# Optimization experiments

Measured on AMD Instinct MI355X. Metric: run time of the kernel, lower is better.

## Reference

```python
import jax, jax.numpy as jnp
import numpy as np

NUM_USERS = 120000
NUM_ITEMS = 30000
NUM_NODES = NUM_USERS + NUM_ITEMS
EMBED_DIM = 64
N_LAYERS = 3
N_EDGES = 4000000


def setup_inputs() -> dict:
    key = jax.random.key(0)
    k_emb, k_row, k_col = jax.random.split(key, 3)
    row = jax.random.randint(k_row, (N_EDGES,), 0, NUM_NODES, dtype=jnp.int32)
    col = jax.random.randint(k_col, (N_EDGES,), 0, NUM_NODES, dtype=jnp.int32)
    # symmetric normalization weights: D^{-1/2}[row] * D^{-1/2}[col]
    deg = jnp.bincount(row, length=NUM_NODES).astype(jnp.float32)
    deg_inv_sqrt = jnp.where(deg > 0, deg ** -0.5, 0.0)
    edge_weight = deg_inv_sqrt[row] * deg_inv_sqrt[col]
    emb = 0.1 * jax.random.normal(k_emb, (NUM_NODES, EMBED_DIM), dtype=jnp.float32)
    return {"emb": emb, "edge_weight": edge_weight, "row": row, "col": col}


def reference(emb, edge_weight, row, col):
    # one LightGCN propagation: out[row] += edge_weight * x[col]  (SpMM)
    def propagate(x):
        msg = x[col] * edge_weight[:, None]            # [E, D] gather + scale
        return jax.ops.segment_sum(msg, row, num_segments=NUM_NODES)  # scatter-add

    out = emb
    xk = emb
    for _ in range(N_LAYERS):
        xk = propagate(xk)
        out = out + xk
    out = out / (N_LAYERS + 1)
    user_emb = out[:NUM_USERS]
    item_emb = out[NUM_USERS:]
    return (user_emb, item_emb)
```

## Files before the change

### kernel.cpp

```cpp
#include <hip/hip_runtime.h>

#define NUM_USERS 120000
#define NUM_ITEMS 30000
#define NUM_NODES 150000
#define EMBED_DIM 64
#define N_LAYERS 3
#define N_EDGES 4000000

#define BW_SHIFT 9
#define BW_ROWS (1 << BW_SHIFT)
#define BW_MASK (BW_ROWS - 1)
#define NBUCK ((NUM_NODES + BW_MASK) >> BW_SHIFT)
#define BUCK_CAP 16000
#define SUB_E 8192

typedef unsigned short us8v __attribute__((ext_vector_type(8)));


__device__ __forceinline__ float bf2f(unsigned short u) {
    union { unsigned int i; float f; } v;
    v.i = ((unsigned int)u) << 16;
    return v.f;
}
__device__ __forceinline__ unsigned short f2bf(float f) {
    union { float f; unsigned int i; } v;
    v.f = f;
    unsigned int u = v.i;
    u += 0x7FFFu + ((u >> 16) & 1u);
    return (unsigned short)(u >> 16);
}


__global__ void zero_ints(int* __restrict__ p, int n) {
    int i = blockIdx.x * blockDim.x + threadIdx.x;
    int stride = gridDim.x * blockDim.x;
    for (; i < n; i += stride) p[i] = 0;
}

__global__ void conv_u0(const float4* __restrict__ emb,
                        const int* __restrict__ rs,
                        ushort4* __restrict__ u0, int n4) {
    int i = blockIdx.x * blockDim.x + threadIdx.x;
    int stride = gridDim.x * blockDim.x;
    for (; i < n4; i += stride) {
        int node = i >> 4;
        int deg = rs[node + 1] - rs[node];
        float dinv = (deg > 0) ? rsqrtf((float)deg) : 0.f;
        float4 v = emb[i];
        ushort4 q;
        q.x = f2bf(v.x * dinv); q.y = f2bf(v.y * dinv);
        q.z = f2bf(v.z * dinv); q.w = f2bf(v.w * dinv);
        u0[i] = q;
    }
}


__global__ void __launch_bounds__(256)
bucket_bin2(const int* __restrict__ row, const int* __restrict__ col,
            int* __restrict__ gcnt, int* __restrict__ stage, int nEdges) {
    __shared__ int lbuf[SUB_E];
    __shared__ int ldst[SUB_E];
    __shared__ int hist[NBUCK];
    __shared__ int cur[NBUCK];
    __shared__ int dlt[NBUCK];
    __shared__ int s0[512], s1[512];

    int nSub = (nEdges + SUB_E - 1) / SUB_E;
    for (int s = blockIdx.x; s < nSub; s += gridDim.x) {
        int e0 = s * SUB_E;
        int n = nEdges - e0; if (n > SUB_E) n = SUB_E;

        for (int j = threadIdx.x; j < NBUCK; j += 256) hist[j] = 0;
        __syncthreads();
        for (int i = threadIdx.x; i < n; i += 256)
            atomicAdd(&hist[row[e0 + i] >> BW_SHIFT], 1);
        __syncthreads();

        for (int j = threadIdx.x; j < 512; j += 256)
            s0[j] = (j < NBUCK) ? hist[j] : 0;
        __syncthreads();
        int *a = s0, *bb = s1;
        for (int off = 1; off < 512; off <<= 1) {
            for (int j = threadIdx.x; j < 512; j += 256) {
                int x = a[j];
                if (j >= off) x += a[j - off];
                bb[j] = x;
            }
            __syncthreads();
            int* t = a; a = bb; bb = t;
        }
        for (int j = threadIdx.x; j < NBUCK; j += 256) {
            int c = hist[j];
            int ls = j ? a[j - 1] : 0;
            cur[j] = ls;
            int g = c ? atomicAdd(&gcnt[j], c) : 0;
            dlt[j] = j * BUCK_CAP + g - ls;
        }
        __syncthreads();
        for (int i = threadIdx.x; i < n; i += 256) {
            int r = row[e0 + i];
            int b = r >> BW_SHIFT;
            int lpos = atomicAdd(&cur[b], 1);
            lbuf[lpos] = ((r & BW_MASK) << 18) | col[e0 + i];
            int d = dlt[b] + lpos;
            ldst[lpos] = (d - b * BUCK_CAP < BUCK_CAP) ? d : -1;
        }
        __syncthreads();
        for (int j = threadIdx.x; j < n; j += 256) {
            int d = ldst[j];
            if (d >= 0) stage[d] = lbuf[j];
        }
        __syncthreads();
    }
}

__global__ void bucket_scan(const int* __restrict__ gcnt, int* __restrict__ bstart,
                            int* __restrict__ rs) {
    __shared__ int s0[512], s1[512];
    int tid = threadIdx.x;
    int v = 0;
    if (tid < NBUCK) { v = gcnt[tid]; if (v > BUCK_CAP) v = BUCK_CAP; }
    s0[tid] = v;
    __syncthreads();
    int* a = s0; int* bb = s1;
    for (int off = 1; off < 512; off <<= 1) {
        int x = a[tid];
        if (tid >= off) x += a[tid - off];
        bb[tid] = x;
        __syncthreads();
        int* t = a; a = bb; bb = t;
    }
    if (tid == 0) bstart[0] = 0;
    if (tid < NBUCK) bstart[tid + 1] = a[tid];
    if (tid == 0) rs[NUM_NODES] = a[NBUCK - 1];
}

__global__ void __launch_bounds__(256)
bucket_scatter(const int* __restrict__ stage, const int* __restrict__ gcnt,
               const int* __restrict__ bstart, int* __restrict__ rs,
               int* __restrict__ csr) {
    __shared__ int s0[BW_ROWS], s1[BW_ROWS];
    int b = blockIdx.x;
    int tid = threadIdx.x;
    int nrec = gcnt[b]; if (nrec > BUCK_CAP) nrec = BUCK_CAP;
    int base = bstart[b];
    const int* st = stage + (size_t)b * BUCK_CAP;
    int baseRow = b << BW_SHIFT;
    int rows = NUM_NODES - baseRow; if (rows > BW_ROWS) rows = BW_ROWS;

    for (int j = tid; j < BW_ROWS; j += 256) s0[j] = 0;
    __syncthreads();
    for (int i = tid; i < nrec; i += 256) atomicAdd(&s0[st[i] >> 18], 1);
    __syncthreads();

    int* a = s0; int* bb = s1;
    for (int off = 1; off < BW_ROWS; off <<= 1) {
        for (int j = tid; j < BW_ROWS; j += 256) {
            int x = a[j];
            if (j >= off) x += a[j - off];
            bb[j] = x;
        }
        __syncthreads();
        int* t = a; a = bb; bb = t;
    }

    for (int r = tid; r < rows; r += 256)
        rs[baseRow + r] = base + (r ? a[r - 1] : 0);

    for (int j = tid; j < BW_ROWS; j += 256) bb[j] = 0;
    __syncthreads();
    for (int i = tid; i < nrec; i += 256) {
        int rec = st[i];
        int r = rec >> 18;
        int rank = atomicAdd(&bb[r], 1);
        csr[base + (r ? a[r - 1] : 0) + rank] = rec & 0x3FFFF;
    }
}

__global__ void __launch_bounds__(256)
lgcn_prop_u(const us8v* __restrict__ xb,
            const int* __restrict__ rs,
            const int* __restrict__ csr,
            us8v* __restrict__ yb, int nNodes) {
    int gtid = blockIdx.x * blockDim.x + threadIdx.x;
    int node = gtid >> 3;
    int sub  = threadIdx.x & 7;
    if (node >= nNodes) return;
    int s = rs[node], e = rs[node + 1];
    float acc[8] = {0.f, 0.f, 0.f, 0.f, 0.f, 0.f, 0.f, 0.f};

    int base = s;
    for (; base + 8 <= e; base += 8) {
        int c8 = csr[base + sub];
        us8v v[8];
#pragma unroll
        for (int j = 0; j < 8; ++j) {
            int bc = __shfl(c8, j, 8);
            v[j] = xb[(size_t)bc * 8 + sub];
        }
#pragma unroll
        for (int j = 0; j < 8; ++j)
#pragma unroll
            for (int k = 0; k < 8; ++k)
                acc[k] += bf2f(v[j][k]);
    }
    if (base < e) {
        int nn = e - base;
        int idx = base + sub;
        int c8 = (idx < e) ? csr[idx] : 0;
        us8v v[7];
#pragma unroll
        for (int j = 0; j < 7; ++j) {
            int bc = __shfl(c8, j, 8);
            v[j] = xb[(size_t)bc * 8 + sub];
        }
#pragma unroll
        for (int j = 0; j < 7; ++j) {
            float m = (j < nn) ? 1.f : 0.f;
#pragma unroll
            for (int k = 0; k < 8; ++k)
                acc[k] = fmaf(bf2f(v[j][k]), m, acc[k]);
        }
    }

    int deg = e - s;
    float dinv = (deg > 0) ? rsqrtf((float)deg) : 0.f;
    float d2 = dinv * dinv;
    us8v q;
#pragma unroll
    for (int k = 0; k < 8; ++k) q[k] = f2bf(acc[k] * d2);
    yb[(size_t)node * 8 + sub] = q;
}

__global__ void lgcn_fuse(const float4* __restrict__ emb,
                          const ushort4* __restrict__ u1,
                          const ushort4* __restrict__ u2,
                          const ushort4* __restrict__ u3,
                          const int* __restrict__ rs,
                          float4* __restrict__ out, int n4) {
    int i = blockIdx.x * blockDim.x + threadIdx.x;
    int stride = gridDim.x * blockDim.x;
    const float quart = 1.0f / (N_LAYERS + 1);
    for (; i < n4; i += stride) {
        int node = i >> 4;
        int deg = rs[node + 1] - rs[node];
        float sd = (deg > 0) ? sqrtf((float)deg) : 0.f;
        ushort4 a = u1[i], b = u2[i], c = u3[i];
        float4 ev = emb[i];
        float4 o;
        o.x = (ev.x + (bf2f(a.x) + bf2f(b.x) + bf2f(c.x)) * sd) * quart;
        o.y = (ev.y + (bf2f(a.y) + bf2f(b.y) + bf2f(c.y)) * sd) * quart;
        o.z = (ev.z + (bf2f(a.z) + bf2f(b.z) + bf2f(c.z)) * sd) * quart;
        o.w = (ev.w + (bf2f(a.w) + bf2f(b.w) + bf2f(c.w)) * sd) * quart;
        out[i] = o;
    }
}


__global__ void lgcn_init(const float4* __restrict__ emb,
                          float4* __restrict__ x,
                          float4* __restrict__ out, int n4) {
    int i = blockIdx.x * blockDim.x + threadIdx.x;
    int stride = gridDim.x * blockDim.x;
    for (; i < n4; i += stride) {
        float4 v = emb[i];
        x[i] = v;
        out[i] = v;
    }
}

__global__ void lgcn_zero(float4* __restrict__ y, int n4) {
    int i = blockIdx.x * blockDim.x + threadIdx.x;
    int stride = gridDim.x * blockDim.x;
    float4 z = make_float4(0.f, 0.f, 0.f, 0.f);
    for (; i < n4; i += stride) y[i] = z;
}

__global__ void lgcn_edge(const float* __restrict__ x,
                          const float* __restrict__ w,
                          const int* __restrict__ row,
                          const int* __restrict__ col,
                          float* __restrict__ y, int nEdges) {
    int tid = blockIdx.x * blockDim.x + threadIdx.x;
    int wave = tid >> 6;
    int lane = threadIdx.x & 63;
    int nWaves = (gridDim.x * blockDim.x) >> 6;
    for (int e = wave; e < nEdges; e += nWaves) {
        int r = row[e];
        int c = col[e];
        float wt = w[e];
        float v = x[(size_t)c * EMBED_DIM + lane] * wt;
        atomicAdd(&y[(size_t)r * EMBED_DIM + lane], v);
    }
}

__global__ void lgcn_accum(const float4* __restrict__ y,
                           float4* __restrict__ out, float scale, int n4) {
    int i = blockIdx.x * blockDim.x + threadIdx.x;
    int stride = gridDim.x * blockDim.x;
    for (; i < n4; i += stride) {
        float4 o = out[i];
        float4 v = y[i];
        o.x = (o.x + v.x) * scale;
        o.y = (o.y + v.y) * scale;
        o.z = (o.z + v.z) * scale;
        o.w = (o.w + v.w) * scale;
        out[i] = o;
    }
}


extern "C" void kernel_launch(void* const* d_in, const int* in_sizes, int n_in,
                              void* d_out, int out_size, void* d_ws, size_t ws_size,
                              hipStream_t stream) {
    const float* emb = (const float*)d_in[0];
    const float* ew  = (const float*)d_in[1];
    const int*   row = (const int*)d_in[2];
    const int*   col = (const int*)d_in[3];
    float* out = (float*)d_out;

    const size_t tableElems = (size_t)NUM_NODES * EMBED_DIM;
    const int n4 = (int)(tableElems / 4);

    char* ws = (char*)d_ws;
    size_t off = 0;
    auto alloc = [&](size_t bytes) {
        char* p = ws + off;
        off += (bytes + 255) & ~(size_t)255;
        return p;
    };
    ushort4* u1b   = (ushort4*)alloc(tableElems * 2);
    ushort4* u2b   = (ushort4*)alloc(tableElems * 2);
    ushort4* u3b   = (ushort4*)alloc(tableElems * 2);
    int*     csr   = (int*)    alloc((size_t)N_EDGES * 4);
    char*    stg0  = alloc(tableElems * 2 > (size_t)NBUCK * BUCK_CAP * 4
                               ? tableElems * 2
                               : (size_t)NBUCK * BUCK_CAP * 4);
    int*     rs    = (int*)    alloc((size_t)(NUM_NODES + 32) * 4);
    int*     bstart= (int*)    alloc((size_t)(NBUCK + 8) * 4);
    int*     gcnt  = (int*)    alloc((size_t)(NBUCK + 8) * 4);
    size_t need = off;
    int*     stage = (int*)stg0;
    ushort4* u0b   = (ushort4*)stg0;

    if (ws_size >= need) {
        zero_ints<<<2, 256, 0, stream>>>(gcnt, NBUCK);
        bucket_bin2<<<512, 256, 0, stream>>>(row, col, gcnt, stage, N_EDGES);
        bucket_scan<<<1, 512, 0, stream>>>(gcnt, bstart, rs);
        bucket_scatter<<<NBUCK, 256, 0, stream>>>(stage, gcnt, bstart, rs, csr);

        conv_u0<<<2048, 256, 0, stream>>>((const float4*)emb, rs,
                                          (ushort4*)u0b, n4);

        const int propBlocks = (NUM_NODES * 8 + 255) / 256;
        lgcn_prop_u<<<propBlocks, 256, 0, stream>>>((const us8v*)u0b, rs, csr,
                                                    (us8v*)u1b, NUM_NODES);
        lgcn_prop_u<<<propBlocks, 256, 0, stream>>>((const us8v*)u1b, rs, csr,
                                                    (us8v*)u2b, NUM_NODES);
        lgcn_prop_u<<<propBlocks, 256, 0, stream>>>((const us8v*)u2b, rs, csr,
                                                    (us8v*)u3b, NUM_NODES);

        lgcn_fuse<<<2048, 256, 0, stream>>>((const float4*)emb,
                                            u1b, u2b, u3b, rs,
                                            (float4*)out, n4);
    } else {
        float* x = (float*)d_ws;
        float* y = x + tableElems;
        lgcn_init<<<2048, 256, 0, stream>>>((const float4*)emb, (float4*)x,
                                            (float4*)out, n4);
        for (int l = 0; l < N_LAYERS; ++l) {
            lgcn_zero<<<2048, 256, 0, stream>>>((float4*)y, n4);
            lgcn_edge<<<4096, 256, 0, stream>>>(x, ew, row, col, y, N_EDGES);
            float scale = (l == N_LAYERS - 1) ? 1.0f / (N_LAYERS + 1) : 1.0f;
            lgcn_accum<<<2048, 256, 0, stream>>>((const float4*)y, (float4*)out,
                                                 scale, n4);
            float* t = x; x = y; y = t;
        }
    }
}
```

Baseline: 336.9 us.

## Fuse bf16 conversion into CSR scatter and final combine into last propagation

Folds the emb-to-bf16 pre-scaling into the bucket_scatter kernel, reusing the per-row degrees already held in shared memory, which removes the separate conv_u0 launch and its extra read of rs. The last propagation layer now computes the final weighted sum of emb, u1, u2 and the fresh layer output directly, which drops the lgcn_fuse kernel and the write and re-read of the u3 table. It also adds a launch_bounds occupancy hint and replaces rsqrt squared with a reciprocal. In exchange, staging no longer aliases u0, so the workspace grows.

Result: no change. 334.1 us (-0.8%).

```diff
diff --git a/kernel.cpp b/kernel.cpp
--- a/kernel.cpp
+++ b/kernel.cpp
@@ -35,23 +35,6 @@
     int i = blockIdx.x * blockDim.x + threadIdx.x;
     int stride = gridDim.x * blockDim.x;
     for (; i < n; i += stride) p[i] = 0;
-}
-
-__global__ void conv_u0(const float4* __restrict__ emb,
-                        const int* __restrict__ rs,
-                        ushort4* __restrict__ u0, int n4) {
-    int i = blockIdx.x * blockDim.x + threadIdx.x;
-    int stride = gridDim.x * blockDim.x;
-    for (; i < n4; i += stride) {
-        int node = i >> 4;
-        int deg = rs[node + 1] - rs[node];
-        float dinv = (deg > 0) ? rsqrtf((float)deg) : 0.f;
-        float4 v = emb[i];
-        ushort4 q;
-        q.x = f2bf(v.x * dinv); q.y = f2bf(v.y * dinv);
-        q.z = f2bf(v.z * dinv); q.w = f2bf(v.w * dinv);
-        u0[i] = q;
-    }
 }
 
 
@@ -138,7 +121,8 @@
 __global__ void __launch_bounds__(256)
 bucket_scatter(const int* __restrict__ stage, const int* __restrict__ gcnt,
                const int* __restrict__ bstart, int* __restrict__ rs,
-               int* __restrict__ csr) {
+               int* __restrict__ csr,
+               const float4* __restrict__ emb4, ushort4* __restrict__ u0) {
     __shared__ int s0[BW_ROWS], s1[BW_ROWS];
     int b = blockIdx.x;
     int tid = threadIdx.x;
@@ -175,13 +159,29 @@
         int rank = atomicAdd(&bb[r], 1);
         csr[base + (r ? a[r - 1] : 0) + rank] = rec & 0x3FFFF;
     }
-}
-
-__global__ void __launch_bounds__(256)
+
+    for (int i = tid; i < rows * 16; i += 256) {
+        int rl = i >> 4;
+        int deg = a[rl] - (rl ? a[rl - 1] : 0);
+        float dinv = (deg > 0) ? rsqrtf((float)deg) : 0.f;
+        int g = baseRow * 16 + i;
+        float4 v = emb4[g];
+        ushort4 q;
+        q.x = f2bf(v.x * dinv); q.y = f2bf(v.y * dinv);
+        q.z = f2bf(v.z * dinv); q.w = f2bf(v.w * dinv);
+        u0[g] = q;
+    }
+}
+
+template <int FINAL>
+__global__ void __launch_bounds__(256, 3)
 lgcn_prop_u(const us8v* __restrict__ xb,
             const int* __restrict__ rs,
             const int* __restrict__ csr,
-            us8v* __restrict__ yb, int nNodes) {
+            us8v* __restrict__ yb,
+            const us8v* __restrict__ u1,
+            const float4* __restrict__ emb,
+            float4* __restrict__ out, int nNodes) {
     int gtid = blockIdx.x * blockDim.x + threadIdx.x;
     int node = gtid >> 3;
     int sub  = threadIdx.x & 7;
@@ -224,35 +224,36 @@
     }
 
     int deg = e - s;
-    float dinv = (deg > 0) ? rsqrtf((float)deg) : 0.f;
-    float d2 = dinv * dinv;
-    us8v q;
-#pragma unroll
-    for (int k = 0; k < 8; ++k) q[k] = f2bf(acc[k] * d2);
-    yb[(size_t)node * 8 + sub] = q;
-}
-
-__global__ void lgcn_fuse(const float4* __restrict__ emb,
-                          const ushort4* __restrict__ u1,
-                          const ushort4* __restrict__ u2,
-                          const ushort4* __restrict__ u3,
-                          const int* __restrict__ rs,
-                          float4* __restrict__ out, int n4) {
-    int i = blockIdx.x * blockDim.x + threadIdx.x;
-    int stride = gridDim.x * blockDim.x;
-    const float quart = 1.0f / (N_LAYERS + 1);
-    for (; i < n4; i += stride) {
-        int node = i >> 4;
-        int deg = rs[node + 1] - rs[node];
+    float d2 = (deg > 0) ? 1.0f / (float)deg : 0.f;
+    size_t o8 = (size_t)node * 8 + sub;
+
+    if (FINAL == 0) {
+        us8v q;
+#pragma unroll
+        for (int k = 0; k < 8; ++k) q[k] = f2bf(acc[k] * d2);
+        yb[o8] = q;
+    } else {
         float sd = (deg > 0) ? sqrtf((float)deg) : 0.f;
-        ushort4 a = u1[i], b = u2[i], c = u3[i];
-        float4 ev = emb[i];
-        float4 o;
-        o.x = (ev.x + (bf2f(a.x) + bf2f(b.x) + bf2f(c.x)) * sd) * quart;
-        o.y = (ev.y + (bf2f(a.y) + bf2f(b.y) + bf2f(c.y)) * sd) * quart;
-        o.z = (ev.z + (bf2f(a.z) + bf2f(b.z) + bf2f(c.z)) * sd) * quart;
-        o.w = (ev.w + (bf2f(a.w) + bf2f(b.w) + bf2f(c.w)) * sd) * quart;
-        out[i] = o;
+        const float quart = 1.0f / (N_LAYERS + 1);
+        us8v a1 = u1[o8];
+        us8v a2 = xb[o8];
+        float sum[8];
+#pragma unroll
+        for (int k = 0; k < 8; ++k)
+            sum[k] = bf2f(a1[k]) + bf2f(a2[k]) + acc[k] * d2;
+        size_t o4 = o8 * 2;
+        float4 e0 = emb[o4], e1 = emb[o4 + 1];
+        float4 r0, r1;
+        r0.x = (e0.x + sum[0] * sd) * quart;
+        r0.y = (e0.y + sum[1] * sd) * quart;
+        r0.z = (e0.z + sum[2] * sd) * quart;
+        r0.w = (e0.w + sum[3] * sd) * quart;
+        r1.x = (e1.x + sum[4] * sd) * quart;
+        r1.y = (e1.y + sum[5] * sd) * quart;
+        r1.z = (e1.z + sum[6] * sd) * quart;
+        r1.w = (e1.w + sum[7] * sd) * quart;
+        out[o4] = r0;
+        out[o4 + 1] = r1;
     }
 }
 
@@ -329,40 +330,33 @@
         off += (bytes + 255) & ~(size_t)255;
         return p;
     };
+    ushort4* u0b   = (ushort4*)alloc(tableElems * 2);
     ushort4* u1b   = (ushort4*)alloc(tableElems * 2);
     ushort4* u2b   = (ushort4*)alloc(tableElems * 2);
-    ushort4* u3b   = (ushort4*)alloc(tableElems * 2);
     int*     csr   = (int*)    alloc((size_t)N_EDGES * 4);
-    char*    stg0  = alloc(tableElems * 2 > (size_t)NBUCK * BUCK_CAP * 4
-                               ? tableElems * 2
-                               : (size_t)NBUCK * BUCK_CAP * 4);
+    int*     stage = (int*)    alloc((size_t)NBUCK * BUCK_CAP * 4);
     int*     rs    = (int*)    alloc((size_t)(NUM_NODES + 32) * 4);
     int*     bstart= (int*)    alloc((size_t)(NBUCK + 8) * 4);
     int*     gcnt  = (int*)    alloc((size_t)(NBUCK + 8) * 4);
     size_t need = off;
-    int*     stage = (int*)stg0;
-    ushort4* u0b   = (ushort4*)stg0;
 
     if (ws_size >= need) {
         zero_ints<<<2, 256, 0, stream>>>(gcnt, NBUCK);
         bucket_bin2<<<512, 256, 0, stream>>>(row, col, gcnt, stage, N_EDGES);
         bucket_scan<<<1, 512, 0, stream>>>(gcnt, bstart, rs);
-        bucket_scatter<<<NBUCK, 256, 0, stream>>>(stage, gcnt, bstart, rs, csr);
-
-        conv_u0<<<2048, 256, 0, stream>>>((const float4*)emb, rs,
-                                          (ushort4*)u0b, n4);
+        bucket_scatter<<<NBUCK, 256, 0, stream>>>(stage, gcnt, bstart, rs, csr,
+                                                  (const float4*)emb, u0b);
 
         const int propBlocks = (NUM_NODES * 8 + 255) / 256;
-        lgcn_prop_u<<<propBlocks, 256, 0, stream>>>((const us8v*)u0b, rs, csr,
-                                                    (us8v*)u1b, NUM_NODES);
-        lgcn_prop_u<<<propBlocks, 256, 0, stream>>>((const us8v*)u1b, rs, csr,
-                                                    (us8v*)u2b, NUM_NODES);
-        lgcn_prop_u<<<propBlocks, 256, 0, stream>>>((const us8v*)u2b, rs, csr,
-                                                    (us8v*)u3b, NUM_NODES);
-
-        lgcn_fuse<<<2048, 256, 0, stream>>>((const float4*)emb,
-                                            u1b, u2b, u3b, rs,
-                                            (float4*)out, n4);
+        lgcn_prop_u<0><<<propBlocks, 256, 0, stream>>>(
+            (const us8v*)u0b, rs, csr, (us8v*)u1b,
+            (const us8v*)u1b, (const float4*)emb, (float4*)out, NUM_NODES);
+        lgcn_prop_u<0><<<propBlocks, 256, 0, stream>>>(
+            (const us8v*)u1b, rs, csr, (us8v*)u2b,
+            (const us8v*)u1b, (const float4*)emb, (float4*)out, NUM_NODES);
+        lgcn_prop_u<1><<<propBlocks, 256, 0, stream>>>(
+            (const us8v*)u2b, rs, csr, (us8v*)u0b,
+            (const us8v*)u1b, (const float4*)emb, (float4*)out, NUM_NODES);
     } else {
         float* x = (float*)d_ws;
         float* y = x + tableElems;
```
